# Kernel tuning notes

Measured on AMD Instinct MI355X. Metric: run time of the kernel, lower is better.

The kernel has to match this reference:

```python
import jax, jax.numpy as jnp
import numpy as np
from jax import lax

B, C = 16, 80
LEVELS = [(100, 128), (50, 64), (25, 32), (13, 16), (7, 8)]
STRIDES = [8, 16, 32, 64, 128]
SCORE_THR = 0.05
IOU_THR = 0.6
MAX_DET = 1000


def make_coords(h, w, stride):
    # FCOS: center of each cell in original-image coordinates, order (x, y)
    ys = jnp.arange(h, dtype=jnp.float32) * stride + stride // 2
    xs = jnp.arange(w, dtype=jnp.float32) * stride + stride // 2
    yy, xx = jnp.meshgrid(ys, xs, indexing='ij')
    return jnp.stack([xx.reshape(-1), yy.reshape(-1)], axis=-1)  # [h*w, 2]


def flatten_levels(feats):
    # list of [B, c, h, w] -> [B, sum(h*w), c]
    return jnp.concatenate(
        [f.transpose(0, 2, 3, 1).reshape(f.shape[0], -1, f.shape[1]) for f in feats], axis=1)


def pairwise_iou(boxes):
    # boxes [N,4]; +1 area convention, matching the torch box_nms
    x1, y1, x2, y2 = boxes[:, 0], boxes[:, 1], boxes[:, 2], boxes[:, 3]
    areas = (x2 - x1 + 1.0) * (y2 - y1 + 1.0)
    xmin = jnp.maximum(x1[:, None], x1[None, :])
    ymin = jnp.maximum(y1[:, None], y1[None, :])
    xmax = jnp.minimum(x2[:, None], x2[None, :])
    ymax = jnp.minimum(y2[:, None], y2[None, :])
    inter = jnp.clip(xmax - xmin, 0.0) * jnp.clip(ymax - ymin, 0.0)
    return inter / (areas[:, None] + areas[None, :] - inter)


def nms_keep_mask(boxes, valid, thr):
    # boxes are sorted by descending score (top_k sorted=True) -> greedy order = index order
    n = boxes.shape[0]
    iou = pairwise_iou(boxes)
    idx = jnp.arange(n)

    def body(i, sup):
        kept = jnp.logical_not(sup[i])
        return sup | (kept & (iou[i] > thr) & (idx > i))

    sup = lax.fori_loop(0, n, body, jnp.logical_not(valid))
    return valid & jnp.logical_not(sup)


def detect_forward(cls_feats, ctr_feats, reg_feats):
    cls_logits = flatten_levels(cls_feats)   # [B, P, C]
    ctr_logits = flatten_levels(ctr_feats)   # [B, P, 1]
    reg_preds = flatten_levels(reg_feats)    # [B, P, 4] (l, t, r, b)
    coords = jnp.concatenate(
        [make_coords(h, w, s) for (h, w), s in zip(LEVELS, STRIDES)], axis=0)  # [P, 2]

    cls_preds = jax.nn.sigmoid(cls_logits)
    ctr_preds = jax.nn.sigmoid(ctr_logits)[..., 0]
    cls_scores = jnp.max(cls_preds, axis=-1) * ctr_preds        # add_centerness=True
    cls_classes = jnp.argmax(cls_preds, axis=-1) + 1            # [B, P] int

    boxes = jnp.concatenate(
        [coords[None] - reg_preds[..., :2], coords[None] + reg_preds[..., 2:]], axis=-1)

    max_num = min(MAX_DET, cls_scores.shape[-1])
    scores_topk, topk_ind = lax.top_k(cls_scores, max_num)      # sorted descending
    classes_topk = jnp.take_along_axis(cls_classes, topk_ind, axis=1)
    boxes_topk = jnp.take_along_axis(boxes, topk_ind[..., None], axis=1)

    valid = scores_topk >= SCORE_THR
    # batched_nms class-offset trick
    max_coord = jnp.max(boxes_topk, axis=(1, 2), keepdims=True)
    offs = classes_topk.astype(boxes_topk.dtype)[..., None] * (max_coord + 1.0)
    boxes_for_nms = boxes_topk + offs

    keep = jax.vmap(lambda b, v: nms_keep_mask(b, v, IOU_THR))(boxes_for_nms, valid)
    keep_f = keep.astype(scores_topk.dtype)
    # fixed-shape masked outputs (torch version returns ragged per-batch lists)
    return scores_topk * keep_f, classes_topk * keep, boxes_topk * keep_f[..., None]


def setup_inputs() -> dict:
    key = jax.random.key(0)
    ks = jax.random.split(key, 3 * len(LEVELS))
    inp = {}
    for i, (h, w) in enumerate(LEVELS):
        inp[f'cls{i}'] = jax.random.normal(ks[3 * i], (B, C, h, w), jnp.float32)
        inp[f'ctr{i}'] = jax.random.normal(ks[3 * i + 1], (B, 1, h, w), jnp.float32)
        # positive ltrb offsets of plausible magnitude
        inp[f'reg{i}'] = jax.random.uniform(ks[3 * i + 2], (B, 4, h, w), jnp.float32) * 64.0 + 1.0
    return inp


def reference(cls0, cls1, cls2, cls3, cls4, ctr0, ctr1, ctr2, ctr3, ctr4,
              reg0, reg1, reg2, reg3, reg4):
    return detect_forward([cls0, cls1, cls2, cls3, cls4],
                          [ctr0, ctr1, ctr2, ctr3, ctr4],
                          [reg0, reg1, reg2, reg3, reg4])
```

## Files before the change

kernel.cpp:

```cpp
#include <hip/hip_runtime.h>
#include <stdint.h>

#define NANCH 17064
#define BATCH 16
#define NCLS 80
#define KDET 1000
#define SCORE_THR 0.05f
#define IOU_THR 0.6f

typedef unsigned long long u64;
typedef unsigned int u32;

__device__ __forceinline__ float sigf(float x) { return 1.0f / (1.0f + expf(-x)); }

__device__ __forceinline__ void decode_anchor(int n, int& l, int& h, int& w) {
  if (n < 12800)      { l = 0; h = n >> 7;               w = n & 127; }
  else if (n < 16000) { l = 1; int r = n - 12800; h = r >> 6; w = r & 63; }
  else if (n < 16800) { l = 2; int r = n - 16000; h = r >> 5; w = r & 31; }
  else if (n < 17008) { l = 3; int r = n - 16800; h = r >> 4; w = r & 15; }
  else                { l = 4; int r = n - 17008; h = r >> 3; w = r & 7; }
}

__device__ __forceinline__ u32 fenc(float f) {
  u32 u = __float_as_uint(f);
  return (u & 0x80000000u) ? ~u : (u | 0x80000000u);
}
__device__ __forceinline__ float fdec(u32 e) {
  u32 u = (e & 0x80000000u) ? (e ^ 0x80000000u) : ~e;
  return __uint_as_float(u);
}

__global__ __launch_bounds__(256) void k_score(
    const float* __restrict__ cls0, const float* __restrict__ ctr0,
    const float* __restrict__ cls1, const float* __restrict__ ctr1,
    const float* __restrict__ cls2, const float* __restrict__ ctr2,
    const float* __restrict__ cls3, const float* __restrict__ ctr3,
    const float* __restrict__ cls4, const float* __restrict__ ctr4,
    u32* __restrict__ sb, u32* __restrict__ cl8)
{
  int q = blockIdx.x * blockDim.x + threadIdx.x;
  if (q >= NANCH / 4) return;
  int b = blockIdx.y;
  int n = q * 4;
  const float* cp; const float* tp; int hw, off;
  if (n < 12800)      { cp = cls0; tp = ctr0; hw = 12800; off = n; }
  else if (n < 16000) { cp = cls1; tp = ctr1; hw = 3200;  off = n - 12800; }
  else if (n < 16800) { cp = cls2; tp = ctr2; hw = 800;   off = n - 16000; }
  else if (n < 17008) { cp = cls3; tp = ctr3; hw = 208;   off = n - 16800; }
  else                { cp = cls4; tp = ctr4; hw = 56;    off = n - 17008; }
  const float4* base = (const float4*)(cp + (size_t)b * NCLS * hw + off);
  const int s4 = hw >> 2;
  float m0 = -1.0f, m1 = -1.0f, m2 = -1.0f, m3 = -1.0f;
  int a0 = 0, a1 = 0, a2 = 0, a3 = 0;
  for (int c = 0; c < NCLS; ++c) {
    float4 v = base[(size_t)c * s4];
    float s0 = sigf(v.x), s1 = sigf(v.y), s2 = sigf(v.z), s3 = sigf(v.w);
    if (s0 > m0) { m0 = s0; a0 = c; }
    if (s1 > m1) { m1 = s1; a1 = c; }
    if (s2 > m2) { m2 = s2; a2 = c; }
    if (s3 > m3) { m3 = s3; a3 = c; }
  }
  float4 ctv = *(const float4*)(tp + (size_t)b * hw + off);
  float c0 = sigf(ctv.x), c1 = sigf(ctv.y), c2 = sigf(ctv.z), c3 = sigf(ctv.w);
  uint4 sv;
  sv.x = __float_as_uint(m0 * c0);
  sv.y = __float_as_uint(m1 * c1);
  sv.z = __float_as_uint(m2 * c2);
  sv.w = __float_as_uint(m3 * c3);
  *(uint4*)(sb + b * NANCH + n) = sv;
  cl8[(b * NANCH + n) >> 2] = (u32)a0 | ((u32)a1 << 8) | ((u32)a2 << 16) | ((u32)a3 << 24);
}

__global__ __launch_bounds__(1024) void k_topk(
    const u32* __restrict__ sb,
    u64* __restrict__ candG, int* __restrict__ cntG, u32* __restrict__ maxcG)
{
  __shared__ u32 hist[1024];
  __shared__ u32 wtot[16];
  __shared__ int s_T1, s_above, s_T2, s_cnt;

  const int tid = threadIdx.x;
  const int b = blockIdx.x;
  const int lane = tid & 63, wv = tid >> 6;
  const u32* sbb = sb + b * NANCH;

  hist[tid] = 0;
  __syncthreads();
  for (int n = tid; n < NANCH; n += 1024) atomicAdd(&hist[sbb[n] >> 22], 1u);
  __syncthreads();
  u32 h = hist[tid];
  u32 s = h;
  for (int d = 1; d < 64; d <<= 1) { u32 y = (u32)__shfl_down((int)s, d); if (lane + d < 64) s += y; }
  if (lane == 0) wtot[wv] = s;
  hist[tid] = 0;
  __syncthreads();
  {
    u32 add = 0;
    for (int w2 = wv + 1; w2 < 16; ++w2) add += wtot[w2];
    s += add;
  }
  if (s >= (u32)KDET && s - h < (u32)KDET) { s_T1 = tid; s_above = (int)(s - h); }
  __syncthreads();
  const int T1 = s_T1; const int above = s_above;

  for (int n = tid; n < NANCH; n += 1024) {
    u32 bits = sbb[n];
    if ((int)(bits >> 22) == T1) atomicAdd(&hist[(bits >> 12) & 1023u], 1u);
  }
  __syncthreads();
  h = hist[tid];
  s = h;
  for (int d = 1; d < 64; d <<= 1) { u32 y = (u32)__shfl_down((int)s, d); if (lane + d < 64) s += y; }
  if (lane == 0) wtot[wv] = s;
  __syncthreads();
  {
    u32 add = 0;
    for (int w2 = wv + 1; w2 < 16; ++w2) add += wtot[w2];
    s += add;
  }
  if (above + (int)s >= KDET && above + (int)(s - h) < KDET) s_T2 = tid;
  if (tid == 0) s_cnt = 0;
  __syncthreads();
  const int T2 = s_T2;

  for (int n = tid; n < NANCH; n += 1024) {
    u32 bits = sbb[n];
    int c1 = (int)(bits >> 22);
    bool cand = (c1 > T1) || (c1 == T1 && (int)((bits >> 12) & 1023u) >= T2);
    if (cand) {
      int pos = atomicAdd(&s_cnt, 1);
      if (pos < 2048) candG[b * 2048 + pos] = ((u64)bits << 32) | (u64)(u32)(~(u32)n);
    }
  }
  __syncthreads();
  if (tid == 0) {
    int C = s_cnt; if (C > 2048) C = 2048;
    cntG[b] = C;
    maxcG[b] = 0u;
  }
}

__global__ __launch_bounds__(256) void k_rank(
    const float* __restrict__ reg0, const float* __restrict__ reg1,
    const float* __restrict__ reg2, const float* __restrict__ reg3,
    const float* __restrict__ reg4,
    const unsigned char* __restrict__ cl8,
    const u64* __restrict__ candG, const int* __restrict__ cntG,
    float* __restrict__ scoreG, int* __restrict__ clsG, float4* __restrict__ boxG,
    u32* __restrict__ maxcG)
{
  __shared__ ulonglong2 keys2[1024];
  const int tid = threadIdx.x;
  const int c = blockIdx.x;
  const int b = blockIdx.y;
  const int lane = tid & 63;
  const int C = cntG[b];
  const u64* cand = candG + b * 2048;

  for (int i = tid; i < 1024; i += 256) {
    int i0 = 2 * i, i1 = 2 * i + 1;
    ulonglong2 v;
    v.x = (i0 < C) ? cand[i0] : 0ull;
    v.y = (i1 < C) ? cand[i1] : 0ull;
    keys2[i] = v;
  }
  __syncthreads();

  const int idx = c * 256 + tid;
  const bool active = (idx < C);
  u64 key = active ? cand[idx] : 0ull;

  int cnt = 0;
  const int Cp2 = ((C + 7) >> 3) << 2;
  for (int s = 0; s < Cp2; s += 4) {
    ulonglong2 a0 = keys2[s], a1 = keys2[s + 1], a2 = keys2[s + 2], a3 = keys2[s + 3];
    cnt += (a0.x > key) + (a0.y > key) + (a1.x > key) + (a1.y > key)
         + (a2.x > key) + (a2.y > key) + (a3.x > key) + (a3.y > key);
  }

  u32 enc = 0u;
  if (active && cnt < KDET) {
    u32 bits = (u32)(key >> 32);
    int n = (int)(~(u32)(key & 0xFFFFFFFFull));
    float score = __uint_as_float(bits);
    int clsv = (int)cl8[b * NANCH + n] + 1;
    int l, hh, ww; decode_anchor(n, l, hh, ww);
    const float* rp; int W, ST, HF, hw;
    switch (l) {
      case 0: rp = reg0; W = 128; ST = 8;   HF = 4;  hw = 12800; break;
      case 1: rp = reg1; W = 64;  ST = 16;  HF = 8;  hw = 3200;  break;
      case 2: rp = reg2; W = 32;  ST = 32;  HF = 16; hw = 800;   break;
      case 3: rp = reg3; W = 16;  ST = 64;  HF = 32; hw = 208;   break;
      default: rp = reg4; W = 8;  ST = 128; HF = 64; hw = 56;    break;
    }
    float cx = (float)(ww * ST + HF);
    float cy = (float)(hh * ST + HF);
    const float* rb = rp + (size_t)b * 4 * hw + hh * W + ww;
    float r0 = rb[0], r1 = rb[hw], r2 = rb[2 * hw], r3 = rb[3 * hw];
    float4 bx = make_float4(cx - r0, cy - r1, cx + r2, cy + r3);
    int o = b * KDET + cnt;
    scoreG[o] = score; clsG[o] = clsv; boxG[o] = bx;
    enc = fenc(fmaxf(fmaxf(bx.x, bx.y), fmaxf(bx.z, bx.w)));
  }
  for (int d = 32; d > 0; d >>= 1) {
    u32 o = (u32)__shfl_xor((int)enc, d);
    enc = (o > enc) ? o : enc;
  }
  if (lane == 0 && enc != 0u) atomicMax(maxcG + b, enc);
}

__global__ __launch_bounds__(256) void k_mat(
    const float4* __restrict__ boxG, const int* __restrict__ clsG,
    const u32* __restrict__ maxcG, u64* __restrict__ mat)
{
  const int tid = threadIdx.x, lane = tid & 63, wv = tid >> 6;
  const int b = blockIdx.y;
  const int tile = blockIdx.x * 4 + wv;
  if (tile >= 136) return;
  int rt = 0, rem = tile;
  while (rem >= rt + 1) { rem -= rt + 1; ++rt; }
  const int wc = rem;

  const float scale = fdec(maxcG[b]) + 1.0f;

  const int j = (wc << 6) + lane;
  float jx1 = 0, jy1 = 0, jx2 = 0, jy2 = 0, aj = 0;
  if (j < KDET) {
    float4 bj = boxG[b * KDET + j];
    float off = (float)clsG[b * KDET + j] * scale;
    jx1 = bj.x + off; jy1 = bj.y + off; jx2 = bj.z + off; jy2 = bj.w + off;
    aj = (jx2 - jx1 + 1.0f) * (jy2 - jy1 + 1.0f);
  }
  const int ri = (rt << 6) + lane;
  float ix1 = 0, iy1 = 0, ix2 = 0, iy2 = 0;
  if (ri < KDET) {
    float4 bi = boxG[b * KDET + ri];
    float off = (float)clsG[b * KDET + ri] * scale;
    ix1 = bi.x + off; iy1 = bi.y + off; ix2 = bi.z + off; iy2 = bi.w + off;
  }

  u64 myword = 0ull;
  for (int r = 0; r < 64; ++r) {
    float x1 = __shfl(ix1, r), y1 = __shfl(iy1, r);
    float x2 = __shfl(ix2, r), y2 = __shfl(iy2, r);
    float ai = (x2 - x1 + 1.0f) * (y2 - y1 + 1.0f);
    int row = (rt << 6) + r;
    float xmin = fmaxf(x1, jx1), ymin = fmaxf(y1, jy1);
    float xmax = fminf(x2, jx2), ymax = fminf(y2, jy2);
    float inter = fmaxf(xmax - xmin, 0.0f) * fmaxf(ymax - ymin, 0.0f);
    float iou = inter / ((ai + aj) - inter);
    bool p = (j < row) && (j < KDET) && (iou > IOU_THR);
    u64 mm = __ballot(p);
    if (lane == r) myword = mm;
  }
  const int rowl = (rt << 6) + lane;
  if (rowl < KDET) mat[(size_t)b * (KDET * 16) + rowl * 16 + wc] = myword;
}

__global__ __launch_bounds__(1024) void k_nms(
    const u64* __restrict__ mat, const float* __restrict__ scoreG,
    const int* __restrict__ clsG, const float4* __restrict__ boxG,
    float* __restrict__ out)
{
  __shared__ u64 keptS[16];
  __shared__ int s_chg;
  const int tid = threadIdx.x;
  const int b = blockIdx.x;
  const int wv = tid >> 6, lane = tid & 63;

  float sc = (tid < KDET) ? scoreG[b * KDET + tid] : 0.0f;
  bool valid = (tid < KDET) && (sc >= SCORE_THR);

  u64 row[16];
  const u64* mrow = mat + (size_t)b * (KDET * 16) + (size_t)tid * 16;
  const int wtop = tid >> 6;
#pragma unroll
  for (int w = 0; w < 16; ++w)
    row[w] = (tid < KDET && w <= wtop) ? mrow[w] : 0ull;

  {
    u64 mb = __ballot(valid);
    if (lane == 0) keptS[wv] = mb;
  }
  __syncthreads();

  for (int it = 0; it < KDET + 1; ++it) {
    u64 sup = 0;
#pragma unroll
    for (int w = 0; w < 16; ++w) sup |= keptS[w] & row[w];
    bool nk = valid && (sup == 0ull);
    u64 nw = __ballot(nk);
    if (tid == 0) s_chg = 0;
    __syncthreads();
    if (lane == 0) {
      if (nw != keptS[wv]) s_chg = 1;
      keptS[wv] = nw;
    }
    __syncthreads();
    if (s_chg == 0) break;
  }

  if (tid < KDET) {
    bool kp = ((keptS[tid >> 6] >> (tid & 63)) & 1ull) != 0ull;
    int o1 = b * KDET + tid;
    out[o1] = kp ? sc : 0.0f;
    out[BATCH * KDET + o1] = kp ? (float)clsG[o1] : 0.0f;
    float4 bx = boxG[o1];
    float* ob = out + 2 * BATCH * KDET + (size_t)o1 * 4;
    ob[0] = kp ? bx.x : 0.0f;
    ob[1] = kp ? bx.y : 0.0f;
    ob[2] = kp ? bx.z : 0.0f;
    ob[3] = kp ? bx.w : 0.0f;
  }
}

extern "C" void kernel_launch(void* const* d_in, const int* in_sizes, int n_in,
                              void* d_out, int out_size, void* d_ws, size_t ws_size,
                              hipStream_t stream) {
  const float* cls[5]; const float* ctr[5]; const float* reg[5];
  for (int i = 0; i < 5; ++i) {
    cls[i] = (const float*)d_in[3 * i + 0];
    ctr[i] = (const float*)d_in[3 * i + 1];
    reg[i] = (const float*)d_in[3 * i + 2];
  }
  char* ws = (char*)d_ws;
  u32* sb   = (u32*)ws;
  unsigned char* cl8 = (unsigned char*)(ws + 1092096);
  u64* candG = (u64*)(ws + 1365120);
  u64* mat  = (u64*)ws;
  float*  scoreG = (float*) (ws + 2048000);
  int*    clsG   = (int*)   (ws + 2112000);
  float4* boxG   = (float4*)(ws + 2176000);
  int*    cntG   = (int*)   (ws + 2432000);
  u32*    maxcG  = (u32*)   (ws + 2432064);

  dim3 g1((NANCH / 4 + 255) / 256, BATCH);
  k_score<<<g1, 256, 0, stream>>>(cls[0], ctr[0], cls[1], ctr[1], cls[2], ctr[2],
                                  cls[3], ctr[3], cls[4], ctr[4], sb, (u32*)cl8);
  k_topk<<<BATCH, 1024, 0, stream>>>(sb, candG, cntG, maxcG);
  k_rank<<<dim3(8, BATCH), 256, 0, stream>>>(reg[0], reg[1], reg[2], reg[3], reg[4],
                                             cl8, candG, cntG, scoreG, clsG, boxG, maxcG);
  k_mat<<<dim3(34, BATCH), 256, 0, stream>>>(boxG, clsG, maxcG, mat);
  k_nms<<<BATCH, 1024, 0, stream>>>(mat, scoreG, clsG, boxG, (float*)d_out);
}
```

Baseline: 235.5 us.

## Split class reduction across four waves per anchor group in k_score

The per-anchor max/argmax over 80 classes is split across four threads (20 classes each), and the partial results are combined through shared memory. The class loop is also unrolled by four so more loads are in flight. This gives the bandwidth-bound first kernel more blocks and more memory-level parallelism, since the old grid was only 17x16 blocks with a serial 80-iteration loop per thread. The cost is a shared-memory reduction, a barrier, and three idle waves during the final combine. Ties still resolve to the lowest class index because partials are merged in ascending order with strict greater-than.

```diff
diff --git a/kernel.cpp b/kernel.cpp
--- a/kernel.cpp
+++ b/kernel.cpp
@@ -38,10 +38,17 @@
     const float* __restrict__ cls4, const float* __restrict__ ctr4,
     u32* __restrict__ sb, u32* __restrict__ cl8)
 {
-  int q = blockIdx.x * blockDim.x + threadIdx.x;
-  if (q >= NANCH / 4) return;
-  int b = blockIdx.y;
-  int n = q * 4;
+  __shared__ float sm[4][64][5];
+  __shared__ u32 sa[4][64];
+
+  const int x = threadIdx.x;
+  const int y = threadIdx.y;
+  const int b = blockIdx.y;
+  int q = blockIdx.x * 64 + x;
+  const bool act = (q < NANCH / 4);
+  int qc = act ? q : (NANCH / 4 - 1);
+  int n = qc * 4;
+
   const float* cp; const float* tp; int hw, off;
   if (n < 12800)      { cp = cls0; tp = ctr0; hw = 12800; off = n; }
   else if (n < 16000) { cp = cls1; tp = ctr1; hw = 3200;  off = n - 12800; }
@@ -50,25 +57,58 @@
   else                { cp = cls4; tp = ctr4; hw = 56;    off = n - 17008; }
   const float4* base = (const float4*)(cp + (size_t)b * NCLS * hw + off);
   const int s4 = hw >> 2;
+
   float m0 = -1.0f, m1 = -1.0f, m2 = -1.0f, m3 = -1.0f;
   int a0 = 0, a1 = 0, a2 = 0, a3 = 0;
-  for (int c = 0; c < NCLS; ++c) {
-    float4 v = base[(size_t)c * s4];
-    float s0 = sigf(v.x), s1 = sigf(v.y), s2 = sigf(v.z), s3 = sigf(v.w);
-    if (s0 > m0) { m0 = s0; a0 = c; }
-    if (s1 > m1) { m1 = s1; a1 = c; }
-    if (s2 > m2) { m2 = s2; a2 = c; }
-    if (s3 > m3) { m3 = s3; a3 = c; }
-  }
-  float4 ctv = *(const float4*)(tp + (size_t)b * hw + off);
-  float c0 = sigf(ctv.x), c1 = sigf(ctv.y), c2 = sigf(ctv.z), c3 = sigf(ctv.w);
-  uint4 sv;
-  sv.x = __float_as_uint(m0 * c0);
-  sv.y = __float_as_uint(m1 * c1);
-  sv.z = __float_as_uint(m2 * c2);
-  sv.w = __float_as_uint(m3 * c3);
-  *(uint4*)(sb + b * NANCH + n) = sv;
-  cl8[(b * NANCH + n) >> 2] = (u32)a0 | ((u32)a1 << 8) | ((u32)a2 << 16) | ((u32)a3 << 24);
+  const int cb = y * 20;
+#pragma unroll
+  for (int cc = 0; cc < 20; cc += 4) {
+    int c = cb + cc;
+    float4 v0 = base[(size_t)(c + 0) * s4];
+    float4 v1 = base[(size_t)(c + 1) * s4];
+    float4 v2 = base[(size_t)(c + 2) * s4];
+    float4 v3 = base[(size_t)(c + 3) * s4];
+    float s;
+    s = sigf(v0.x); if (s > m0) { m0 = s; a0 = c; }
+    s = sigf(v0.y); if (s > m1) { m1 = s; a1 = c; }
+    s = sigf(v0.z); if (s > m2) { m2 = s; a2 = c; }
+    s = sigf(v0.w); if (s > m3) { m3 = s; a3 = c; }
+    s = sigf(v1.x); if (s > m0) { m0 = s; a0 = c + 1; }
+    s = sigf(v1.y); if (s > m1) { m1 = s; a1 = c + 1; }
+    s = sigf(v1.z); if (s > m2) { m2 = s; a2 = c + 1; }
+    s = sigf(v1.w); if (s > m3) { m3 = s; a3 = c + 1; }
+    s = sigf(v2.x); if (s > m0) { m0 = s; a0 = c + 2; }
+    s = sigf(v2.y); if (s > m1) { m1 = s; a1 = c + 2; }
+    s = sigf(v2.z); if (s > m2) { m2 = s; a2 = c + 2; }
+    s = sigf(v2.w); if (s > m3) { m3 = s; a3 = c + 2; }
+    s = sigf(v3.x); if (s > m0) { m0 = s; a0 = c + 3; }
+    s = sigf(v3.y); if (s > m1) { m1 = s; a1 = c + 3; }
+    s = sigf(v3.z); if (s > m2) { m2 = s; a2 = c + 3; }
+    s = sigf(v3.w); if (s > m3) { m3 = s; a3 = c + 3; }
+  }
+  sm[y][x][0] = m0; sm[y][x][1] = m1; sm[y][x][2] = m2; sm[y][x][3] = m3;
+  sa[y][x] = (u32)a0 | ((u32)a1 << 8) | ((u32)a2 << 16) | ((u32)a3 << 24);
+  __syncthreads();
+
+  if (y == 0 && act) {
+#pragma unroll
+    for (int k = 1; k < 4; ++k) {
+      u32 pk = sa[k][x];
+      float t;
+      t = sm[k][x][0]; if (t > m0) { m0 = t; a0 = (int)(pk & 0xffu); }
+      t = sm[k][x][1]; if (t > m1) { m1 = t; a1 = (int)((pk >> 8) & 0xffu); }
+      t = sm[k][x][2]; if (t > m2) { m2 = t; a2 = (int)((pk >> 16) & 0xffu); }
+      t = sm[k][x][3]; if (t > m3) { m3 = t; a3 = (int)((pk >> 24) & 0xffu); }
+    }
+    float4 ctv = *(const float4*)(tp + (size_t)b * hw + off);
+    uint4 sv;
+    sv.x = __float_as_uint(m0 * sigf(ctv.x));
+    sv.y = __float_as_uint(m1 * sigf(ctv.y));
+    sv.z = __float_as_uint(m2 * sigf(ctv.z));
+    sv.w = __float_as_uint(m3 * sigf(ctv.w));
+    *(uint4*)(sb + b * NANCH + n) = sv;
+    cl8[(b * NANCH + n) >> 2] = (u32)a0 | ((u32)a1 << 8) | ((u32)a2 << 16) | ((u32)a3 << 24);
+  }
 }
 
 __global__ __launch_bounds__(1024) void k_topk(
@@ -334,9 +374,9 @@
   int*    cntG   = (int*)   (ws + 2432000);
   u32*    maxcG  = (u32*)   (ws + 2432064);
 
-  dim3 g1((NANCH / 4 + 255) / 256, BATCH);
-  k_score<<<g1, 256, 0, stream>>>(cls[0], ctr[0], cls[1], ctr[1], cls[2], ctr[2],
-                                  cls[3], ctr[3], cls[4], ctr[4], sb, (u32*)cl8);
+  dim3 g1((NANCH / 4 + 63) / 64, BATCH);
+  k_score<<<g1, dim3(64, 4), 0, stream>>>(cls[0], ctr[0], cls[1], ctr[1], cls[2], ctr[2],
+                                          cls[3], ctr[3], cls[4], ctr[4], sb, (u32*)cl8);
   k_topk<<<BATCH, 1024, 0, stream>>>(sb, candG, cntG, maxcG);
   k_rank<<<dim3(8, BATCH), 256, 0, stream>>>(reg[0], reg[1], reg[2], reg[3], reg[4],
                                              cl8, candG, cntG, scoreG, clsG, boxG, maxcG);
```

Measured after the change: 197.8 us. 16.0% less time.
